# Kernel optimization log

Measured on AMD Instinct MI355X. Metric: run time of the kernel, lower is better.

## Reference

```python
import jax, jax.numpy as jnp
import numpy as np

B, T, C = 2, 2048, 1024
NH, H = 16, 64
FF = 3 * C  # feedforward_factor = 3
EPS = 1e-6


def setup_inputs() -> dict:
    key = jax.random.key(0)
    ks = jax.random.split(key, 12)
    s = lambda k, shape, fan: jax.random.normal(k, shape, jnp.float32) * (fan ** -0.5)
    return {
        "x":  jax.random.normal(ks[0], (B, T, C), jnp.float32),
        # per-head projections, stored [nh, C, H] (torch Linear weight [H,C] transposed)
        "Wq": s(ks[1], (NH, C, H), C),
        "Wk": s(ks[2], (NH, C, H), C),
        "Wv": s(ks[3], (NH, C, H), C),
        # combine_heads: torch Linear(nh*H -> C): weight [C, nh*H], bias [C]
        "Wo": s(ks[4], (C, NH * H), NH * H),
        "bo": jnp.zeros((C,), jnp.float32),
        # feedforward
        "W1": s(ks[5], (FF, C), C),
        "b1": jnp.zeros((FF,), jnp.float32),
        "W2": s(ks[6], (C, FF), FF),
        "b2": jnp.zeros((C,), jnp.float32),
        # layer norms (affine)
        "g1": jnp.ones((C,), jnp.float32),
        "be1": jnp.zeros((C,), jnp.float32),
        "g2": jnp.ones((C,), jnp.float32),
        "be2": jnp.zeros((C,), jnp.float32),
    }


def _layernorm(x, gamma, beta):
    # torch: mean / unbiased std (ddof=1), eps added to std (not variance)
    mean = jnp.mean(x, axis=-1, keepdims=True)
    std = jnp.std(x, axis=-1, keepdims=True, ddof=1)
    return gamma * (x - mean) / (std + EPS) + beta


def _attention(xn, Wq, Wk, Wv, Wo, bo):
    q = jnp.einsum("btc,hck->bhtk", xn, Wq)
    k = jnp.einsum("bsc,hck->bhsk", xn, Wk)
    v = jnp.einsum("bsc,hck->bhsk", xn, Wv)
    scores = jnp.einsum("bhtk,bhsk->bhts", q, k) / jnp.sqrt(jnp.float32(H))
    causal = jnp.tril(jnp.ones((T, T), dtype=bool))
    scores = jnp.where(causal, scores, -jnp.inf)
    attn = jax.nn.softmax(scores, axis=-1)
    ctx = jnp.einsum("bhts,bhsk->bhtk", attn, v)
    ctx = jnp.transpose(ctx, (0, 2, 1, 3)).reshape(xn.shape[0], T, NH * H)
    return ctx @ Wo.T + bo


def reference(x, Wq, Wk, Wv, Wo, bo, W1, b1, W2, b2, g1, be1, g2, be2):
    x = x + _attention(_layernorm(x, g1, be1), Wq, Wk, Wv, Wo, bo)
    h = _layernorm(x, g2, be2)
    x = x + (jax.nn.relu(h @ W1.T + b1) @ W2.T + b2)
    return x
```

## Files before the change

### kernel.cpp

```cpp
#include <hip/hip_runtime.h>
#include <stdint.h>

#define Tn   2048
#define Cn   1024
#define NHn  16
#define Hn   64
#define FFn  3072
#define Mrows 4096
#define LNEPS 1e-6f

#if __has_builtin(__builtin_amdgcn_exp2f)
#define EXP2(x) __builtin_amdgcn_exp2f(x)
#else
#define EXP2(x) exp2f(x)
#endif

typedef float f32x4 __attribute__((ext_vector_type(4)));
typedef __bf16 bf16x8 __attribute__((ext_vector_type(8)));
typedef unsigned short us8 __attribute__((ext_vector_type(8)));
typedef unsigned short us4 __attribute__((ext_vector_type(4)));
typedef unsigned int u32x4 __attribute__((ext_vector_type(4)));
typedef unsigned int u32x2 __attribute__((ext_vector_type(2)));

__device__ __forceinline__ unsigned short f2bf(float f) {
    return __builtin_bit_cast(unsigned short, (__bf16)f);
}

__device__ __forceinline__ uint32_t pk2bf(float lo, float hi) {
    return (uint32_t)f2bf(lo) | ((uint32_t)f2bf(hi) << 16);
}

__device__ __forceinline__ void gl_lds16(const void* g, void* l) {
    __builtin_amdgcn_global_load_lds(
        (const __attribute__((address_space(1))) void*)g,
        (__attribute__((address_space(3))) void*)l, 16, 0, 0);
}

__global__ __launch_bounds__(256) void cast_qkv_kernel(
    const float* __restrict__ Wq, const float* __restrict__ Wk,
    const float* __restrict__ Wv, unsigned short* __restrict__ out)
{
    int idx = blockIdx.x * 256 + threadIdx.x;
    int n = idx >> 10, cc = idx & 1023;
    const float* W = (n < 1024) ? Wq : ((n < 2048) ? Wk : Wv);
    int nn = n & 1023;
    float v = W[(size_t)((nn >> 6) * 1024 + cc) * 64 + (nn & 63)];
    out[idx] = f2bf(v);
}

__global__ __launch_bounds__(256) void cast_w_kernel(
    const float* __restrict__ src, unsigned short* __restrict__ dst, int count)
{
    int idx = blockIdx.x * 256 + threadIdx.x;
    if (idx < count) dst[idx] = f2bf(src[idx]);
}

__global__ __launch_bounds__(256) void ln_kernel(
    const float* __restrict__ xin, const float* __restrict__ gamma,
    const float* __restrict__ beta, unsigned short* __restrict__ out)
{
    const int row = blockIdx.x;
    const int tid = threadIdx.x;
    const float4 v = ((const float4*)(xin + (size_t)row * Cn))[tid];
    float s  = v.x + v.y + v.z + v.w;
    float ss = v.x*v.x + v.y*v.y + v.z*v.z + v.w*v.w;
    #pragma unroll
    for (int off = 1; off < 64; off <<= 1) {
        s  += __shfl_xor(s, off);
        ss += __shfl_xor(ss, off);
    }
    __shared__ float red[8];
    const int wave = tid >> 6, lane = tid & 63;
    if (lane == 0) { red[wave] = s; red[4 + wave] = ss; }
    __syncthreads();
    float S  = red[0] + red[1] + red[2] + red[3];
    float SS = red[4] + red[5] + red[6] + red[7];
    float mean = S * (1.0f / 1024.0f);
    float var  = (SS - 1024.0f * mean * mean) * (1.0f / 1023.0f);
    var = fmaxf(var, 0.0f);
    float inv = 1.0f / (sqrtf(var) + LNEPS);
    const float4 gv = ((const float4*)gamma)[tid];
    const float4 bv = ((const float4*)beta)[tid];
    us4 ov;
    ov[0] = f2bf(gv.x * (v.x - mean) * inv + bv.x);
    ov[1] = f2bf(gv.y * (v.y - mean) * inv + bv.y);
    ov[2] = f2bf(gv.z * (v.z - mean) * inv + bv.z);
    ov[3] = f2bf(gv.w * (v.w - mean) * inv + bv.w);
    *(us4*)(out + (size_t)row * Cn + tid * 4) = ov;
}

template<int MODE>
__global__ __launch_bounds__(512) void gemm_bt(
    const unsigned short* __restrict__ A,
    const unsigned short* __restrict__ Bt,
    void* Cout,
    const float* __restrict__ bias,
    const float* resid,
    int M, int N, int K)
{
    __shared__ unsigned short lds[3][8192];
    const int tid  = threadIdx.x;
    const int wave = tid >> 6, lane = tid & 63;
    const int g = lane >> 4, c = lane & 15;
    const int wr = wave >> 2, wc = wave & 3;
    const int m0 = blockIdx.x * 128, n0 = blockIdx.y * 128;

    f32x4 acc[4][2];
    #pragma unroll
    for (int i = 0; i < 4; i++)
        #pragma unroll
        for (int j = 0; j < 2; j++) acc[i][j] = (f32x4){0.f, 0.f, 0.f, 0.f};

    const int srow = wave * 16 + (lane >> 2);
    const int scol = (lane & 3) * 8;
    const unsigned short* sA = A  + (size_t)(m0 + srow) * K + scol;
    const unsigned short* sB = Bt + (size_t)(n0 + srow) * K + scol;
    const int wdst = wave * 512;

    auto STAGE = [&](int t, int b) {
        const int ko = t * 32;
        gl_lds16(sA + ko, &lds[b][wdst]);
        gl_lds16(sB + ko, &lds[b][4096 + wdst]);
    };

    STAGE(0, 0);
    STAGE(1, 1);
    asm volatile("s_waitcnt vmcnt(2)" ::: "memory");
    __builtin_amdgcn_s_barrier();

    const int NT = K >> 5;
    int cur = 0;
    for (int t = 0; t < NT; ++t) {
        const bool pf = (t + 2 < NT);
        if (pf) { int b = cur + 2; if (b >= 3) b -= 3; STAGE(t + 2, b); }

        bf16x8 af[4], bfr[2];
        #pragma unroll
        for (int mi = 0; mi < 4; mi++)
            af[mi]  = *(const bf16x8*)&lds[cur][(wr * 64 + mi * 16 + c) * 32 + g * 8];
        #pragma unroll
        for (int ni = 0; ni < 2; ni++)
            bfr[ni] = *(const bf16x8*)&lds[cur][4096 + (wc * 32 + ni * 16 + c) * 32 + g * 8];
        __builtin_amdgcn_s_setprio(1);
        #pragma unroll
        for (int mi = 0; mi < 4; mi++)
            #pragma unroll
            for (int ni = 0; ni < 2; ni++)
                acc[mi][ni] = __builtin_amdgcn_mfma_f32_16x16x32_bf16(
                    af[mi], bfr[ni], acc[mi][ni], 0, 0, 0);
        __builtin_amdgcn_s_setprio(0);

        if (pf) asm volatile("s_waitcnt vmcnt(2)" ::: "memory");
        else    asm volatile("s_waitcnt vmcnt(0)" ::: "memory");
        __builtin_amdgcn_s_barrier();
        cur = (cur == 2) ? 0 : cur + 1;
    }

    const int rowb = m0 + wr * 64 + g * 4;
    const int colb = n0 + wc * 32 + c;
    #pragma unroll
    for (int mi = 0; mi < 4; mi++) {
        #pragma unroll
        for (int ni = 0; ni < 2; ni++) {
            const int col = colb + ni * 16;
            float bv = (MODE == 1 || MODE == 2) ? bias[col] : 0.f;
            #pragma unroll
            for (int r = 0; r < 4; r++) {
                const int row = rowb + mi * 16 + r;
                float v = acc[mi][ni][r];
                if (MODE == 1) {
                    float res = resid[(size_t)row * N + col];
                    ((float*)Cout)[(size_t)row * N + col] = v + bv + res;
                } else if (MODE == 2) {
                    float t = v + bv;
                    t = t > 0.f ? t : 0.f;
                    ((unsigned short*)Cout)[(size_t)row * N + col] = f2bf(t);
                } else {
                    ((unsigned short*)Cout)[(size_t)row * N + col] = f2bf(v);
                }
            }
        }
    }
}

__global__ __launch_bounds__(256) void transpose_v_kernel(
    const unsigned short* __restrict__ qkv, unsigned short* __restrict__ vt)
{
    __shared__ unsigned short tile[64][72];
    const int bh = blockIdx.y;
    const int b = bh >> 4, h = bh & 15;
    const int t0 = blockIdx.x * 64;
    const int tid = threadIdx.x;
    const int tr = tid >> 2;
    const int dc = (tid & 3) * 16;
    const unsigned short* src =
        qkv + (size_t)(b * Tn + t0 + tr) * 3072 + 2048 + h * 64 + dc;
    *(us8*)&tile[tr][dc]     = *(const us8*)src;
    *(us8*)&tile[tr][dc + 8] = *(const us8*)(src + 8);
    __syncthreads();
    const int dr = tid >> 2;
    const int tc = (tid & 3) * 16;
    unsigned short* dst = vt + (size_t)bh * Hn * Tn + (size_t)dr * Tn + t0 + tc;
    us8 o0, o1;
    #pragma unroll
    for (int e = 0; e < 8; e++) o0[e] = tile[tc + e][dr];
    #pragma unroll
    for (int e = 0; e < 8; e++) o1[e] = tile[tc + 8 + e][dr];
    *(us8*)dst       = o0;
    *(us8*)(dst + 8) = o1;
}

__global__ __launch_bounds__(128, 2) void attn_kernel(
    const unsigned short* __restrict__ qkv,
    const unsigned short* __restrict__ vt,
    unsigned short* __restrict__ ctx)
{
    const float SCL = 0.125f * 1.44269504088896f;
    __shared__ float Osh[2][4][64][4];
    __shared__ float Msh[2][64];
    __shared__ float Lsh[2][64];
    __shared__ uint32_t Psh[2][2][16][36];

    const int tid  = threadIdx.x;
    const int wave = tid >> 6, lane = tid & 63;
    const int g = lane >> 4, c = lane & 15;
    const int l = blockIdx.x;
    const int pj = l >> 5;
    const int bh = ((l & 7) << 2) | ((l >> 3) & 3);
    const int b = bh >> 4, h = bh & 15;
    const unsigned short* base  = qkv + (size_t)b * Tn * 3072;
    const unsigned short* qbase = base + h * 64;
    const unsigned short* kbase = base + 1024 + h * 64;
    const unsigned short* vtb   = vt + (size_t)bh * (Hn * Tn);

    for (int half = 0; half < 2; ++half) {
        const int tileIdx = half ? (63 - pj) : pj;
        const int t0 = tileIdx * 32;
        const int nch  = (t0 + 95) >> 6;
        const int nh0  = (nch + 1) >> 1;
        const int cbeg = wave ? nh0 : 0;
        const int cend = wave ? nch : nh0;

        bf16x8 qf[2][2];
        #pragma unroll
        for (int qa = 0; qa < 2; qa++) {
            const unsigned short* qp = qbase + (size_t)(t0 + qa * 16 + c) * 3072 + g * 8;
            qf[qa][0] = *(const bf16x8*)qp;
            qf[qa][1] = *(const bf16x8*)(qp + 32);
        }

        float mrun[2] = {-1e30f, -1e30f};
        float lrun[2] = {0.f, 0.f};
        f32x4 o[2][4];
        #pragma unroll
        for (int qa = 0; qa < 2; qa++)
            #pragma unroll
            for (int nc = 0; nc < 4; nc++) o[qa][nc] = (f32x4){0.f, 0.f, 0.f, 0.f};

        for (int ci = cbeg; ci < cend; ++ci) {
            const int s0 = ci * 64;
            bf16x8 kf[4][2];
            #pragma unroll
            for (int sc = 0; sc < 4; sc++) {
                const unsigned short* kp = kbase + (size_t)(s0 + sc * 16 + c) * 3072 + g * 8;
                kf[sc][0] = *(const bf16x8*)kp;
                kf[sc][1] = *(const bf16x8*)(kp + 32);
            }
            bf16x8 vf[4][2];
            #pragma unroll
            for (int nc = 0; nc < 4; nc++)
                #pragma unroll
                for (int ks = 0; ks < 2; ks++)
                    vf[nc][ks] = *(const bf16x8*)(vtb + (size_t)(nc * 16 + c) * Tn
                                                  + s0 + ks * 32 + g * 8);

            f32x4 sacc[2][4];
            #pragma unroll
            for (int qa = 0; qa < 2; qa++)
                #pragma unroll
                for (int sc = 0; sc < 4; sc++) {
                    f32x4 z = (f32x4){0.f, 0.f, 0.f, 0.f};
                    z = __builtin_amdgcn_mfma_f32_16x16x32_bf16(kf[sc][0], qf[qa][0], z, 0, 0, 0);
                    z = __builtin_amdgcn_mfma_f32_16x16x32_bf16(kf[sc][1], qf[qa][1], z, 0, 0, 0);
                    sacc[qa][sc] = z;
                }

            uint32_t dw[2][4][2];
            #pragma unroll
            for (int qa = 0; qa < 2; qa++) {
                const int q = t0 + qa * 16 + c;
                float pm[4][4];
                const bool needMask = (s0 + 63 > t0 + qa * 16);
                #pragma unroll
                for (int sc = 0; sc < 4; sc++)
                    #pragma unroll
                    for (int r = 0; r < 4; r++) {
                        float v = sacc[qa][sc][r] * SCL;
                        if (needMask && (s0 + sc * 16 + 4 * g + r > q)) v = -1e30f;
                        pm[sc][r] = v;
                    }
                float tmax = pm[0][0];
                #pragma unroll
                for (int sc = 0; sc < 4; sc++)
                    #pragma unroll
                    for (int r = 0; r < 4; r++) tmax = fmaxf(tmax, pm[sc][r]);
                tmax = fmaxf(tmax, __shfl_xor(tmax, 16));
                tmax = fmaxf(tmax, __shfl_xor(tmax, 32));
                float mnew = fmaxf(mrun[qa], tmax);
                float corr = EXP2(mrun[qa] - mnew);
                mrun[qa] = mnew;
                float csum = 0.f;
                #pragma unroll
                for (int sc = 0; sc < 4; sc++)
                    #pragma unroll
                    for (int r = 0; r < 4; r++) {
                        float p = EXP2(pm[sc][r] - mnew);
                        pm[sc][r] = p;
                        csum += p;
                    }
                csum += __shfl_xor(csum, 16);
                csum += __shfl_xor(csum, 32);
                lrun[qa] = lrun[qa] * corr + csum;
                float cb[4];
                #pragma unroll
                for (int r = 0; r < 4; r++) cb[r] = __shfl(corr, 4 * g + r);
                #pragma unroll
                for (int nc = 0; nc < 4; nc++)
                    #pragma unroll
                    for (int r = 0; r < 4; r++) o[qa][nc][r] *= cb[r];
                #pragma unroll
                for (int sc = 0; sc < 4; sc++) {
                    dw[qa][sc][0] = pk2bf(pm[sc][0], pm[sc][1]);
                    dw[qa][sc][1] = pk2bf(pm[sc][2], pm[sc][3]);
                }
            }

            #pragma unroll
            for (int qa = 0; qa < 2; qa++)
                #pragma unroll
                for (int sc = 0; sc < 4; sc++) {
                    u32x2 wv = { dw[qa][sc][0], dw[qa][sc][1] };
                    *(u32x2*)&Psh[wave][qa][c][sc * 8 + 2 * g] = wv;
                }
            #pragma unroll
            for (int ks = 0; ks < 2; ks++) {
                #pragma unroll
                for (int qa = 0; qa < 2; qa++) {
                    u32x4 pd = *(const u32x4*)&Psh[wave][qa][c][ks * 16 + 4 * g];
                    bf16x8 pa = __builtin_bit_cast(bf16x8, pd);
                    #pragma unroll
                    for (int nc = 0; nc < 4; nc++)
                        o[qa][nc] = __builtin_amdgcn_mfma_f32_16x16x32_bf16(
                            pa, vf[nc][ks], o[qa][nc], 0, 0, 0);
                }
            }
        }

        f32x4 oS[4], oX[4];
        float mS, lS, mX, lX;
        if (wave == 0) {
            #pragma unroll
            for (int nc = 0; nc < 4; nc++) { oS[nc] = o[0][nc]; oX[nc] = o[1][nc]; }
            mS = mrun[0]; lS = lrun[0]; mX = mrun[1]; lX = lrun[1];
        } else {
            #pragma unroll
            for (int nc = 0; nc < 4; nc++) { oS[nc] = o[1][nc]; oX[nc] = o[0][nc]; }
            mS = mrun[1]; lS = lrun[1]; mX = mrun[0]; lX = lrun[0];
        }
        #pragma unroll
        for (int nc = 0; nc < 4; nc++)
            *(f32x4*)&Osh[wave][nc][lane][0] = oX[nc];
        Msh[wave][lane] = mX;
        Lsh[wave][lane] = lX;
        __syncthreads();
        const int pw = wave ^ 1;
        float mP = Msh[pw][lane];
        float lP = Lsh[pw][lane];
        float mM = fmaxf(mS, mP);
        float cS = EXP2(mS - mM);
        float cP = EXP2(mP - mM);
        float rl = 1.0f / (lS * cS + lP * cP);
        float cbS[4], cbP[4], lb[4];
        #pragma unroll
        for (int r = 0; r < 4; r++) {
            cbS[r] = __shfl(cS, 4 * g + r);
            cbP[r] = __shfl(cP, 4 * g + r);
            lb[r]  = __shfl(rl, 4 * g + r);
        }
        #pragma unroll
        for (int nc = 0; nc < 4; nc++) {
            f32x4 oP = *(const f32x4*)&Osh[pw][nc][lane][0];
            #pragma unroll
            for (int r = 0; r < 4; r++) {
                const int trow = t0 + wave * 16 + 4 * g + r;
                float val = (oS[nc][r] * cbS[r] + oP[r] * cbP[r]) * lb[r];
                ctx[(size_t)(b * Tn + trow) * 1024 + h * 64 + nc * 16 + c] = f2bf(val);
            }
        }
        __syncthreads();
    }
}

extern "C" void kernel_launch(void* const* d_in, const int* in_sizes, int n_in,
                              void* d_out, int out_size, void* d_ws, size_t ws_size,
                              hipStream_t stream) {
    const float* x   = (const float*)d_in[0];
    const float* Wq  = (const float*)d_in[1];
    const float* Wk  = (const float*)d_in[2];
    const float* Wv  = (const float*)d_in[3];
    const float* Wo  = (const float*)d_in[4];
    const float* bo  = (const float*)d_in[5];
    const float* W1  = (const float*)d_in[6];
    const float* b1  = (const float*)d_in[7];
    const float* W2  = (const float*)d_in[8];
    const float* b2  = (const float*)d_in[9];
    const float* g1  = (const float*)d_in[10];
    const float* be1 = (const float*)d_in[11];
    const float* g2  = (const float*)d_in[12];
    const float* be2 = (const float*)d_in[13];

    char* ws = (char*)d_ws;
    unsigned short* wqkv = (unsigned short*)ws;  ws += (size_t)3072 * 1024 * 2;
    unsigned short* wo   = (unsigned short*)ws;  ws += (size_t)1024 * 1024 * 2;
    unsigned short* w1   = (unsigned short*)ws;  ws += (size_t)3072 * 1024 * 2;
    unsigned short* w2   = (unsigned short*)ws;  ws += (size_t)1024 * 3072 * 2;
    unsigned short* bufA = (unsigned short*)ws;  ws += (size_t)Mrows * 1024 * 2;
    unsigned short* bufB = (unsigned short*)ws;  ws += (size_t)Mrows * 3072 * 2;

    float* xout = (float*)d_out;
    unsigned short* vt = (unsigned short*)d_out;

    cast_qkv_kernel<<<12288, 256, 0, stream>>>(Wq, Wk, Wv, wqkv);
    cast_w_kernel<<<4096, 256, 0, stream>>>(Wo, wo, 1024 * 1024);
    cast_w_kernel<<<12288, 256, 0, stream>>>(W1, w1, 3072 * 1024);
    cast_w_kernel<<<12288, 256, 0, stream>>>(W2, w2, 1024 * 3072);

    ln_kernel<<<Mrows, 256, 0, stream>>>(x, g1, be1, bufA);
    gemm_bt<0><<<dim3(32, 24), 512, 0, stream>>>(bufA, wqkv, bufB, nullptr, nullptr,
                                                 Mrows, 3072, 1024);
    transpose_v_kernel<<<dim3(Tn / 64, 2 * NHn), 256, 0, stream>>>(bufB, vt);
    attn_kernel<<<dim3(1024), 128, 0, stream>>>(bufB, vt, bufA);
    gemm_bt<1><<<dim3(32, 8), 512, 0, stream>>>(bufA, wo, xout, bo, x,
                                                Mrows, 1024, 1024);
    ln_kernel<<<Mrows, 256, 0, stream>>>(xout, g2, be2, bufA);
    gemm_bt<2><<<dim3(32, 24), 512, 0, stream>>>(bufA, w1, bufB, b1, nullptr,
                                                 Mrows, 3072, 1024);
    gemm_bt<1><<<dim3(32, 8), 512, 0, stream>>>(bufB, w2, xout, b2, (const float*)xout,
                                                Mrows, 1024, 3072);
}
```

Baseline: 244.9 us.

## Restructure GEMM into split-K waves with 64-deep K tiles and swizzled LDS

```diff
diff --git a/kernel.cpp b/kernel.cpp
--- a/kernel.cpp
+++ b/kernel.cpp
@@ -90,7 +90,7 @@
 }
 
 template<int MODE>
-__global__ __launch_bounds__(512) void gemm_bt(
+__global__ __launch_bounds__(512, 4) void gemm_bt(
     const unsigned short* __restrict__ A,
     const unsigned short* __restrict__ Bt,
     void* Cout,
@@ -98,85 +98,111 @@
     const float* resid,
     int M, int N, int K)
 {
-    __shared__ unsigned short lds[3][8192];
+    __shared__ unsigned short lds[2][16384];
     const int tid  = threadIdx.x;
     const int wave = tid >> 6, lane = tid & 63;
     const int g = lane >> 4, c = lane & 15;
-    const int wr = wave >> 2, wc = wave & 3;
+    const int wk = wave >> 2, wr = (wave >> 1) & 1, wc = wave & 1;
     const int m0 = blockIdx.x * 128, n0 = blockIdx.y * 128;
 
-    f32x4 acc[4][2];
+    f32x4 acc[4][4];
     #pragma unroll
     for (int i = 0; i < 4; i++)
         #pragma unroll
-        for (int j = 0; j < 2; j++) acc[i][j] = (f32x4){0.f, 0.f, 0.f, 0.f};
-
-    const int srow = wave * 16 + (lane >> 2);
-    const int scol = (lane & 3) * 8;
-    const unsigned short* sA = A  + (size_t)(m0 + srow) * K + scol;
-    const unsigned short* sB = Bt + (size_t)(n0 + srow) * K + scol;
-    const int wdst = wave * 512;
+        for (int j = 0; j < 4; j++) acc[i][j] = (f32x4){0.f, 0.f, 0.f, 0.f};
+
+    const int srow  = wave * 8 + (lane >> 3);
+    const int sunit = (lane & 7) ^ ((lane >> 3) & 7);
+    const unsigned short* sA0 = A  + (size_t)(m0 + srow)      * K + sunit * 8;
+    const unsigned short* sA1 = A  + (size_t)(m0 + 64 + srow) * K + sunit * 8;
+    const unsigned short* sB0 = Bt + (size_t)(n0 + srow)      * K + sunit * 8;
+    const unsigned short* sB1 = Bt + (size_t)(n0 + 64 + srow) * K + sunit * 8;
+    const int wdst = (wave * 64 + lane) * 8;
 
     auto STAGE = [&](int t, int b) {
-        const int ko = t * 32;
-        gl_lds16(sA + ko, &lds[b][wdst]);
-        gl_lds16(sB + ko, &lds[b][4096 + wdst]);
+        const int ko = t * 64;
+        gl_lds16(sA0 + ko, &lds[b][wdst]);
+        gl_lds16(sA1 + ko, &lds[b][4096 + wdst]);
+        gl_lds16(sB0 + ko, &lds[b][8192 + wdst]);
+        gl_lds16(sB1 + ko, &lds[b][12288 + wdst]);
     };
 
     STAGE(0, 0);
-    STAGE(1, 1);
-    asm volatile("s_waitcnt vmcnt(2)" ::: "memory");
+    asm volatile("s_waitcnt vmcnt(0)" ::: "memory");
     __builtin_amdgcn_s_barrier();
 
-    const int NT = K >> 5;
+    const int jsw = ((wk * 4 + g) ^ (c & 7)) * 8;
+
+    const int NT = K >> 6;
     int cur = 0;
     for (int t = 0; t < NT; ++t) {
-        const bool pf = (t + 2 < NT);
-        if (pf) { int b = cur + 2; if (b >= 3) b -= 3; STAGE(t + 2, b); }
-
-        bf16x8 af[4], bfr[2];
+        const bool pf = (t + 1 < NT);
+        if (pf) STAGE(t + 1, cur ^ 1);
+
+        bf16x8 af[4], bfr[4];
         #pragma unroll
         for (int mi = 0; mi < 4; mi++)
-            af[mi]  = *(const bf16x8*)&lds[cur][(wr * 64 + mi * 16 + c) * 32 + g * 8];
-        #pragma unroll
-        for (int ni = 0; ni < 2; ni++)
-            bfr[ni] = *(const bf16x8*)&lds[cur][4096 + (wc * 32 + ni * 16 + c) * 32 + g * 8];
+            af[mi]  = *(const bf16x8*)&lds[cur][(wr * 64 + mi * 16 + c) * 64 + jsw];
+        #pragma unroll
+        for (int ni = 0; ni < 4; ni++)
+            bfr[ni] = *(const bf16x8*)&lds[cur][8192 + (wc * 64 + ni * 16 + c) * 64 + jsw];
         __builtin_amdgcn_s_setprio(1);
         #pragma unroll
         for (int mi = 0; mi < 4; mi++)
             #pragma unroll
-            for (int ni = 0; ni < 2; ni++)
+            for (int ni = 0; ni < 4; ni++)
                 acc[mi][ni] = __builtin_amdgcn_mfma_f32_16x16x32_bf16(
                     af[mi], bfr[ni], acc[mi][ni], 0, 0, 0);
         __builtin_amdgcn_s_setprio(0);
 
-        if (pf) asm volatile("s_waitcnt vmcnt(2)" ::: "memory");
-        else    asm volatile("s_waitcnt vmcnt(0)" ::: "memory");
+        if (pf) asm volatile("s_waitcnt vmcnt(0)" ::: "memory");
         __builtin_amdgcn_s_barrier();
-        cur = (cur == 2) ? 0 : cur + 1;
+        cur ^= 1;
     }
 
-    const int rowb = m0 + wr * 64 + g * 4;
-    const int colb = n0 + wc * 32 + c;
-    #pragma unroll
-    for (int mi = 0; mi < 4; mi++) {
-        #pragma unroll
-        for (int ni = 0; ni < 2; ni++) {
-            const int col = colb + ni * 16;
-            float bv = (MODE == 1 || MODE == 2) ? bias[col] : 0.f;
-            #pragma unroll
-            for (int r = 0; r < 4; r++) {
-                const int row = rowb + mi * 16 + r;
-                float v = acc[mi][ni][r];
-                if (MODE == 1) {
-                    float res = resid[(size_t)row * N + col];
-                    ((float*)Cout)[(size_t)row * N + col] = v + bv + res;
-                } else if (MODE == 2) {
-                    float t = v + bv;
-                    t = t > 0.f ? t : 0.f;
-                    ((unsigned short*)Cout)[(size_t)row * N + col] = f2bf(t);
-                } else {
-                    ((unsigned short*)Cout)[(size_t)row * N + col] = f2bf(v);
+    float* mb = (float*)&lds[0][0];
+    const int q = wr * 2 + wc;
+    if (wk == 1) {
+        #pragma unroll
+        for (int mi = 0; mi < 4; mi++)
+            #pragma unroll
+            for (int ni = 0; ni < 4; ni++)
+                #pragma unroll
+                for (int r = 0; r < 4; r++)
+                    mb[q * 4096 + (mi * 16 + g * 4 + r) * 64 + ni * 16 + c] = acc[mi][ni][r];
+    }
+    __syncthreads();
+    if (wk == 0) {
+        #pragma unroll
+        for (int mi = 0; mi < 4; mi++)
+            #pragma unroll
+            for (int ni = 0; ni < 4; ni++)
+                #pragma unroll
+                for (int r = 0; r < 4; r++)
+                    acc[mi][ni][r] += mb[q * 4096 + (mi * 16 + g * 4 + r) * 64 + ni * 16 + c];
+
+        const int rowb = m0 + wr * 64 + g * 4;
+        const int colb = n0 + wc * 64 + c;
+        #pragma unroll
+        for (int mi = 0; mi < 4; mi++) {
+            #pragma unroll
+            for (int ni = 0; ni < 4; ni++) {
+                const int col = colb + ni * 16;
+                float bv = (MODE == 1 || MODE == 2) ? bias[col] : 0.f;
+                #pragma unroll
+                for (int r = 0; r < 4; r++) {
+                    const int row = rowb + mi * 16 + r;
+                    float v = acc[mi][ni][r];
+                    if (MODE == 1) {
+                        float res = resid[(size_t)row * N + col];
+                        ((float*)Cout)[(size_t)row * N + col] = v + bv + res;
+                    } else if (MODE == 2) {
+                        float t = v + bv;
+                        t = t > 0.f ? t : 0.f;
+                        ((unsigned short*)Cout)[(size_t)row * N + col] = f2bf(t);
+                    } else {
+                        ((unsigned short*)Cout)[(size_t)row * N + col] = f2bf(v);
+                    }
                 }
             }
         }
```

After: 249.8 us. 2.0% more time.
